# Kernel optimization log

Hardware: AMD Instinct MI355X
Metric: run time of the kernel (lower is better)

Reference implementation:

```python
import jax, jax.numpy as jnp
import numpy as np

# model geometry (matches init_kwargs cfg)
D = 768        # D_EMB
PATCH = 16
T = 8192
N = T // PATCH # 512 patch tokens
H = 12         # heads
HD = D // H    # 64 head dim
NL = 6         # layers
DFF = 4 * D
B = 8
LN_EPS = 1e-5


def setup_inputs() -> dict:
    key = jax.random.key(0)
    ks = iter(jax.random.split(key, 32))
    def g(shape, scale=0.02):
        return jax.random.normal(next(ks), shape, jnp.float32) * scale
    return dict(
        x=jax.random.normal(next(ks), (B, T), jnp.float32),
        pp_w=g((D, PATCH)), pp_b=jnp.zeros((D,), jnp.float32),
        pe=g((N, D)),
        ln1_g=jnp.ones((NL, D), jnp.float32), ln1_b=jnp.zeros((NL, D), jnp.float32),
        qkv_w=g((NL, 3 * D, D)), out_w=g((NL, D, D)),
        ln2_g=jnp.ones((NL, D), jnp.float32), ln2_b=jnp.zeros((NL, D), jnp.float32),
        fc1_w=g((NL, DFF, D)), fc2_w=g((NL, D, DFF)),
        lnf_g=jnp.ones((D,), jnp.float32), lnf_b=jnp.zeros((D,), jnp.float32),
        h1_w=g((D // 2, D)), h1_b=jnp.zeros((D // 2,), jnp.float32),
        h2_w=g((2, D // 2)), h2_b=jnp.zeros((2,), jnp.float32),
    )


def _ln(x, g, b):
    m = x.mean(-1, keepdims=True)
    v = ((x - m) ** 2).mean(-1, keepdims=True)
    return (x - m) / jnp.sqrt(v + LN_EPS) * g + b


def reference(x, pp_w, pp_b, pe, ln1_g, ln1_b, qkv_w, out_w,
              ln2_g, ln2_b, fc1_w, fc2_w, lnf_g, lnf_b,
              h1_w, h1_b, h2_w, h2_b):
    Bx = x.shape[0]
    # patch embed: [B, N, PATCH] @ W^T + b -> [B, N, D]
    z = jnp.einsum('bnp,dp->bnd', x[:, :N * PATCH].reshape(Bx, N, PATCH), pp_w) + pp_b
    z = z + pe  # positional embedding (arange indexes whole table)
    mask = jnp.tril(jnp.ones((N, N), dtype=bool))
    for i in range(NL):
        # --- attention (manual causal softmax, dropout=eval/no-op) ---
        h = _ln(z, ln1_g[i], ln1_b[i])
        qkv = jnp.einsum('bnd,ed->bne', h, qkv_w[i])            # [B,N,3D]
        qkv = qkv.reshape(Bx, N, 3, H, HD).transpose(2, 0, 3, 1, 4)
        q, k, v = qkv[0], qkv[1], qkv[2]                         # [B,H,N,HD]
        s = jnp.einsum('bhld,bhmd->bhlm', q, k) / np.sqrt(HD)
        s = jnp.where(mask, s, -jnp.inf)
        a = jax.nn.softmax(s, axis=-1)
        o = jnp.einsum('bhlm,bhmd->bhld', a, v)
        o = o.transpose(0, 2, 1, 3).reshape(Bx, N, D)
        z = z + jnp.einsum('bnd,ed->bne', o, out_w[i])
        # --- FFN (exact gelu, matching F.gelu default) ---
        h = _ln(z, ln2_g[i], ln2_b[i])
        f = jax.nn.gelu(jnp.einsum('bnd,fd->bnf', h, fc1_w[i]), approximate=False)
        z = z + jnp.einsum('bnf,df->bnd', f, fc2_w[i])
    enc = _ln(z, lnf_g, lnf_b).mean(axis=1)                      # [B, D]
    y = jax.nn.relu(enc @ h1_w.T + h1_b)
    return y @ h2_w.T + h2_b                                     # [B, 2]
```

## Files before the change

kernel.cpp:

```cpp
#include <hip/hip_runtime.h>
#include <hip/hip_bf16.h>
#include <math.h>

#define D_EMB 768
#define NPATCH 16
#define NTOK 512
#define NHEAD 12
#define HDIM 64
#define NLAYER 6
#define DFF 3072
#define BATCH 8
#define MTOK (BATCH * NTOK)

typedef __attribute__((ext_vector_type(8))) short bf16x8;
typedef __attribute__((ext_vector_type(8))) ushort u16x8;
typedef __attribute__((ext_vector_type(4))) float f32x4;

__device__ __forceinline__ float bf2f(ushort s) {
    unsigned u = ((unsigned)s) << 16;
    return __builtin_bit_cast(float, u);
}
__device__ __forceinline__ ushort f2bf(float f) {
    unsigned u = __builtin_bit_cast(unsigned, f);
    unsigned r = (u + 0x7FFFu + ((u >> 16) & 1u)) >> 16;
    return (ushort)r;
}

__global__ __launch_bounds__(256)
void f2bf4_kernel(const float* __restrict__ s0, ushort* __restrict__ d0, int n0,
                  const float* __restrict__ s1, ushort* __restrict__ d1, int n1,
                  const float* __restrict__ s2, ushort* __restrict__ d2, int n2,
                  const float* __restrict__ s3, ushort* __restrict__ d3, int n3)
{
    int i = blockIdx.x * 256 + threadIdx.x;
    const float* s; ushort* d; long long off;
    if (i < n0)                { s = s0; d = d0; off = i; }
    else if (i < n0 + n1)      { s = s1; d = d1; off = i - n0; }
    else if (i < n0 + n1 + n2) { s = s2; d = d2; off = i - n0 - n1; }
    else if (i < n0 + n1 + n2 + n3) { s = s3; d = d3; off = i - n0 - n1 - n2; }
    else return;
    float4 v0 = *(const float4*)(s + off * 8);
    float4 v1 = *(const float4*)(s + off * 8 + 4);
    u16x8 o;
    o[0] = f2bf(v0.x); o[1] = f2bf(v0.y); o[2] = f2bf(v0.z); o[3] = f2bf(v0.w);
    o[4] = f2bf(v1.x); o[5] = f2bf(v1.y); o[6] = f2bf(v1.z); o[7] = f2bf(v1.w);
    *(u16x8*)(d + off * 8) = o;
}

__global__ __launch_bounds__(256)
void patch_embed_kernel(const float* __restrict__ x, const float* __restrict__ pw,
                        const float* __restrict__ pb, const float* __restrict__ pe,
                        float* __restrict__ z)
{
    int bn = blockIdx.x;
    int b = bn >> 9, n = bn & 511;
    __shared__ float xs[NPATCH];
    int t = threadIdx.x;
    if (t < NPATCH) xs[t] = x[(size_t)b * 8192 + n * NPATCH + t];
    __syncthreads();
    for (int d = t; d < D_EMB; d += 256) {
        float acc = pb[d] + pe[(size_t)n * D_EMB + d];
        const float* w = pw + (size_t)d * NPATCH;
        #pragma unroll
        for (int p = 0; p < NPATCH; ++p) acc += xs[p] * w[p];
        z[(size_t)bn * D_EMB + d] = acc;
    }
}

__device__ __forceinline__ float block_reduce_sum_256(float v)
{
    __shared__ float lds[4];
    #pragma unroll
    for (int o = 32; o > 0; o >>= 1) v += __shfl_xor(v, o);
    int lane = threadIdx.x & 63, wid = threadIdx.x >> 6;
    __syncthreads();
    if (lane == 0) lds[wid] = v;
    __syncthreads();
    return lds[0] + lds[1] + lds[2] + lds[3];
}

__device__ __forceinline__ void store_val(float* p, float v)  { *p = v; }
__device__ __forceinline__ void store_val(ushort* p, float v) { *p = f2bf(v); }

template<typename OT>
__global__ __launch_bounds__(256)
void ln_kernel(const float* __restrict__ x, const float* __restrict__ g,
               const float* __restrict__ bta, OT* __restrict__ y)
{
    int row = blockIdx.x;
    const float* xr = x + (size_t)row * D_EMB;
    int t = threadIdx.x;
    float vals[3];
    float s = 0.f;
    #pragma unroll
    for (int i = 0; i < 3; ++i) { vals[i] = xr[t + i * 256]; s += vals[i]; }
    float mean = block_reduce_sum_256(s) * (1.0f / D_EMB);
    float ss = 0.f;
    #pragma unroll
    for (int i = 0; i < 3; ++i) { float d = vals[i] - mean; ss += d * d; }
    float var = block_reduce_sum_256(ss) * (1.0f / D_EMB);
    float rstd = rsqrtf(var + 1e-5f);
    #pragma unroll
    for (int i = 0; i < 3; ++i) {
        int d = t + i * 256;
        store_val(y + (size_t)row * D_EMB + d, (vals[i] - mean) * rstd * g[d] + bta[d]);
    }
}

template<typename OT>
__global__ __launch_bounds__(256)
void reduce_ln_kernel(const float* __restrict__ pbuf, float* __restrict__ z,
                      const float* __restrict__ g, const float* __restrict__ bta,
                      OT* __restrict__ y)
{
    int row = blockIdx.x;
    int t = threadIdx.x;
    const float* p0 = pbuf + (size_t)row * D_EMB;
    const float* p1 = pbuf + (size_t)MTOK * D_EMB + (size_t)row * D_EMB;
    float* zr = z + (size_t)row * D_EMB;
    float vals[3];
    float s = 0.f;
    #pragma unroll
    for (int i = 0; i < 3; ++i) {
        int d = t + i * 256;
        float v = zr[d] + p0[d] + p1[d];
        vals[i] = v;
        zr[d] = v;
        s += v;
    }
    float mean = block_reduce_sum_256(s) * (1.0f / D_EMB);
    float ss = 0.f;
    #pragma unroll
    for (int i = 0; i < 3; ++i) { float d = vals[i] - mean; ss += d * d; }
    float var = block_reduce_sum_256(ss) * (1.0f / D_EMB);
    float rstd = rsqrtf(var + 1e-5f);
    #pragma unroll
    for (int i = 0; i < 3; ++i) {
        int d = t + i * 256;
        store_val(y + (size_t)row * D_EMB + d, (vals[i] - mean) * rstd * g[d] + bta[d]);
    }
}

#define STAGE64(buf)                                                               \
    {                                                                              \
        _Pragma("unroll")                                                          \
        for (int j = 0; j < 2; ++j) {                                              \
            __builtin_amdgcn_global_load_lds(                                      \
                (const __attribute__((address_space(1))) unsigned int*)gA[j],      \
                (__attribute__((address_space(3))) unsigned int*)&As[buf][dA[j]],  \
                16, 0, 0);                                                         \
            gA[j] += 64;                                                           \
        }                                                                          \
        _Pragma("unroll")                                                          \
        for (int j = 0; j < 4; ++j) {                                              \
            __builtin_amdgcn_global_load_lds(                                      \
                (const __attribute__((address_space(1))) unsigned int*)gB[j],      \
                (__attribute__((address_space(3))) unsigned int*)&Bs[buf][dB[j]],  \
                16, 0, 0);                                                         \
            gB[j] += 64;                                                           \
        }                                                                          \
    }

#define COMPUTE64(buf)                                                             \
    {                                                                              \
        bf16x8 a0[4], a1[4], b0[2], b1[2];                                         \
        _Pragma("unroll")                                                          \
        for (int m = 0; m < 4; ++m) {                                              \
            a0[m] = *(const bf16x8*)(&As[buf][rA[m] + x0]);                        \
            a1[m] = *(const bf16x8*)(&As[buf][rA[m] + x1]);                        \
        }                                                                          \
        _Pragma("unroll")                                                          \
        for (int n = 0; n < 2; ++n) {                                              \
            b0[n] = *(const bf16x8*)(&Bs[buf][rB[n] + x0]);                        \
            b1[n] = *(const bf16x8*)(&Bs[buf][rB[n] + x1]);                        \
        }                                                                          \
        _Pragma("unroll")                                                          \
        for (int m = 0; m < 4; ++m)                                                \
            _Pragma("unroll")                                                      \
            for (int n = 0; n < 2; ++n)                                            \
                acc[m][n] = __builtin_amdgcn_mfma_f32_16x16x32_bf16(a0[m], b0[n], acc[m][n], 0, 0, 0); \
        _Pragma("unroll")                                                          \
        for (int m = 0; m < 4; ++m)                                                \
            _Pragma("unroll")                                                      \
            for (int n = 0; n < 2; ++n)                                            \
                acc[m][n] = __builtin_amdgcn_mfma_f32_16x16x32_bf16(a1[m], b1[n], acc[m][n], 0, 0, 0); \
    }

template<int EPI, typename OT, bool SPLITK>
__global__ __launch_bounds__(256)
void mfma_gemm(const ushort* __restrict__ A, const ushort* __restrict__ W,
               OT* __restrict__ C, const float* __restrict__ res,
               int N, int K, int lda)
{
    __shared__ ushort As[2][64 * 64];
    __shared__ ushort Bs[2][128 * 64];

    int gx = gridDim.x, gy = gridDim.y;
    int bx = blockIdx.x, by = blockIdx.y;
    int bz = SPLITK ? blockIdx.z : 0;
    if ((gy & 7) == 0) {
        int flat = bx + gx * (by + gy * bz);
        int xcd = flat & 7, j = flat >> 3;
        int ry = gy >> 3;
        by = xcd * ry + (j % ry);
        int rem = j / ry;
        bx = rem % gx;
        bz = rem / gx;
    }
    int bm = by * 64, bn = bx * 128;

    const ushort* Ab = A + (size_t)bz * K;
    const ushort* Wb = W + (size_t)bz * K;
    OT* Cb = C + (SPLITK ? (size_t)bz * ((size_t)gy * 64) * N : 0);

    int tid = threadIdx.x;
    int w = tid >> 6, l = tid & 63;
    int lr = l & 15, lg = l >> 4;
    f32x4 acc[4][2] = {};

    int srow = w * 8 + (l >> 3);
    int pcol = l & 7;
    int lcol8 = (pcol ^ (srow & 7)) << 3;

    const ushort* gA[2]; const ushort* gB[4];
    int dA[2], dB[4];
    #pragma unroll
    for (int j = 0; j < 2; ++j) {
        gA[j] = Ab + (size_t)(bm + j * 32 + srow) * lda + lcol8;
        dA[j] = (j * 32 + srow) * 64 + (pcol << 3);
    }
    #pragma unroll
    for (int j = 0; j < 4; ++j) {
        gB[j] = Wb + (size_t)(bn + j * 32 + srow) * lda + lcol8;
        dB[j] = (j * 32 + srow) * 64 + (pcol << 3);
    }

    int x0 = ((lg ^ (lr & 7)) << 3);
    int x1 = (((4 + lg) ^ (lr & 7)) << 3);
    int rA[4], rB[2];
    #pragma unroll
    for (int m = 0; m < 4; ++m) rA[m] = (m * 16 + lr) * 64;
    #pragma unroll
    for (int n = 0; n < 2; ++n) rB[n] = (w * 32 + n * 16 + lr) * 64;

    const int nk = K >> 6;
    STAGE64(0);
    __syncthreads();
    for (int t = 0; t < nk; t += 2) {
        STAGE64(1);
        COMPUTE64(0);
        __syncthreads();
        if (t + 2 < nk) STAGE64(0);
        COMPUTE64(1);
        __syncthreads();
    }

    int r0 = lg * 4;
    #pragma unroll
    for (int m = 0; m < 4; ++m) {
        #pragma unroll
        for (int n = 0; n < 2; ++n) {
            #pragma unroll
            for (int j = 0; j < 4; ++j) {
                int gm = bm + m * 16 + r0 + j;
                int gn = bn + w * 32 + n * 16 + lr;
                float v = acc[m][n][j];
                if (EPI == 1) v = 0.5f * v * (1.0f + erff(v * 0.70710678118654752f));
                if (EPI == 2) v += res[(size_t)gm * N + gn];
                store_val(Cb + (size_t)gm * N + gn, v);
            }
        }
    }
}

__global__ __launch_bounds__(256)
void attn_mfma_kernel(const ushort* __restrict__ qkv, ushort* __restrict__ o)
{
    int w = threadIdx.x >> 6, l = threadIdx.x & 63;
    int qt = blockIdx.x * 4 + w;
    int h = blockIdx.y, b = blockIdx.z;
    int q0 = qt * 16;
    int lr = l & 15, lg = l >> 4;

    const size_t rs = 3 * D_EMB;
    const ushort* qbase = qkv + ((size_t)(b * NTOK)) * rs + h * HDIM;
    const ushort* kbase = qbase + D_EMB;
    const ushort* vbase = qbase + 2 * D_EMB;

    bf16x8 qf[2];
    qf[0] = *(const bf16x8*)(qbase + (size_t)(q0 + lr) * rs + lg * 8);
    qf[1] = *(const bf16x8*)(qbase + (size_t)(q0 + lr) * rs + 32 + lg * 8);

    f32x4 oacc[4] = {};
    float m_j[4], l_j[4];
    #pragma unroll
    for (int j = 0; j < 4; ++j) { m_j[j] = -1e30f; l_j[j] = 0.f; }

    __shared__ ushort P_lds[4][16][40];

    int ntiles = q0 / 32 + 1;
    for (int mt = 0; mt < ntiles; ++mt) {
        int m0 = mt * 32;
        f32x4 s[2] = {};
        #pragma unroll
        for (int kb = 0; kb < 2; ++kb) {
            const ushort* kr = kbase + (size_t)(m0 + kb * 16 + lr) * rs;
            bf16x8 k0 = *(const bf16x8*)(kr + lg * 8);
            bf16x8 k1 = *(const bf16x8*)(kr + 32 + lg * 8);
            s[kb] = __builtin_amdgcn_mfma_f32_16x16x32_bf16(qf[0], k0, s[kb], 0, 0, 0);
            s[kb] = __builtin_amdgcn_mfma_f32_16x16x32_bf16(qf[1], k1, s[kb], 0, 0, 0);
        }
        bool partial = (m0 + 31 > q0);
        float p[2][4], mx[4];
        #pragma unroll
        for (int j = 0; j < 4; ++j) {
            int qr = q0 + lg * 4 + j;
            float s0 = s[0][j] * 0.125f;
            float s1 = s[1][j] * 0.125f;
            if (partial) {
                if (m0 + lr > qr)      s0 = -1e30f;
                if (m0 + 16 + lr > qr) s1 = -1e30f;
            }
            p[0][j] = s0; p[1][j] = s1;
            float mm = fmaxf(s0, s1);
            mm = fmaxf(mm, __shfl_xor(mm, 1));
            mm = fmaxf(mm, __shfl_xor(mm, 2));
            mm = fmaxf(mm, __shfl_xor(mm, 4));
            mm = fmaxf(mm, __shfl_xor(mm, 8));
            mx[j] = mm;
        }
        #pragma unroll
        for (int j = 0; j < 4; ++j) {
            float mnew = fmaxf(m_j[j], mx[j]);
            float scale = __expf(m_j[j] - mnew);
            float p0 = __expf(p[0][j] - mnew);
            float p1 = __expf(p[1][j] - mnew);
            p[0][j] = p0; p[1][j] = p1;
            float rsum = p0 + p1;
            rsum += __shfl_xor(rsum, 1);
            rsum += __shfl_xor(rsum, 2);
            rsum += __shfl_xor(rsum, 4);
            rsum += __shfl_xor(rsum, 8);
            l_j[j] = l_j[j] * scale + rsum;
            m_j[j] = mnew;
            #pragma unroll
            for (int i = 0; i < 4; ++i) oacc[i][j] *= scale;
        }
        #pragma unroll
        for (int kb = 0; kb < 2; ++kb)
            #pragma unroll
            for (int j = 0; j < 4; ++j)
                P_lds[w][lg * 4 + j][kb * 16 + lr] = f2bf(p[kb][j]);
        asm volatile("s_waitcnt lgkmcnt(0)" ::: "memory");
        bf16x8 pa = *(const bf16x8*)(&P_lds[w][lr][lg * 8]);
        #pragma unroll
        for (int i = 0; i < 4; ++i) {
            bf16x8 vf;
            const ushort* vp = vbase + (size_t)(m0 + lg * 8) * rs + i * 16 + lr;
            #pragma unroll
            for (int j = 0; j < 8; ++j) vf[j] = (short)vp[(size_t)j * rs];
            oacc[i] = __builtin_amdgcn_mfma_f32_16x16x32_bf16(pa, vf, oacc[i], 0, 0, 0);
        }
    }
    #pragma unroll
    for (int i = 0; i < 4; ++i) {
        #pragma unroll
        for (int j = 0; j < 4; ++j) {
            int qr = q0 + lg * 4 + j;
            int d  = i * 16 + lr;
            float v = oacc[i][j] / l_j[j];
            o[((size_t)(b * NTOK + qr)) * D_EMB + h * HDIM + d] = f2bf(v);
        }
    }
}

__global__ void mean_kernel(const float* __restrict__ x, float* __restrict__ enc)
{
    int b = blockIdx.x; int d = threadIdx.x;
    float s = 0.f;
    for (int n = 0; n < NTOK; ++n) s += x[((size_t)(b * NTOK + n)) * D_EMB + d];
    enc[b * D_EMB + d] = s * (1.0f / NTOK);
}

__global__ void head1_kernel(const float* __restrict__ enc, const float* __restrict__ w,
                             const float* __restrict__ bias, float* __restrict__ r)
{
    int b = blockIdx.x; int j = threadIdx.x;
    float acc = bias[j];
    const float* e = enc + b * D_EMB;
    const float* wr = w + (size_t)j * D_EMB;
    for (int k = 0; k < D_EMB; ++k) acc += e[k] * wr[k];
    r[b * 384 + j] = fmaxf(acc, 0.f);
}

__global__ void head2_kernel(const float* __restrict__ r, const float* __restrict__ w,
                             const float* __restrict__ bias, float* __restrict__ out)
{
    int idx = threadIdx.x;
    if (idx >= 16) return;
    int b = idx >> 1, j = idx & 1;
    float acc = bias[j];
    for (int k = 0; k < 384; ++k) acc += r[b * 384 + k] * w[j * 384 + k];
    out[b * 2 + j] = acc;
}

extern "C" void kernel_launch(void* const* d_in, const int* in_sizes, int n_in,
                              void* d_out, int out_size, void* d_ws, size_t ws_size,
                              hipStream_t stream)
{
    const float* x     = (const float*)d_in[0];
    const float* pp_w  = (const float*)d_in[1];
    const float* pp_b  = (const float*)d_in[2];
    const float* pe    = (const float*)d_in[3];
    const float* ln1_g = (const float*)d_in[4];
    const float* ln1_b = (const float*)d_in[5];
    const float* qkv_w = (const float*)d_in[6];
    const float* out_w = (const float*)d_in[7];
    const float* ln2_g = (const float*)d_in[8];
    const float* ln2_b = (const float*)d_in[9];
    const float* fc1_w = (const float*)d_in[10];
    const float* fc2_w = (const float*)d_in[11];
    const float* lnf_g = (const float*)d_in[12];
    const float* lnf_b = (const float*)d_in[13];
    const float* h1_w  = (const float*)d_in[14];
    const float* h1_b  = (const float*)d_in[15];
    const float* h2_w  = (const float*)d_in[16];
    const float* h2_b  = (const float*)d_in[17];
    float* out = (float*)d_out;

    const int nq = 3 * D_EMB * D_EMB, no = D_EMB * D_EMB, nf = DFF * D_EMB;
    const size_t per_layer_w = ((size_t)nq + no + 2 * nf) * 2;

    char* p = (char*)d_ws;
    float*  z      = (float*)p;  p += (size_t)MTOK * D_EMB * 4;
    ushort* big_bf = (ushort*)p; p += (size_t)MTOK * DFF * 2;
    ushort* h_bf   = (ushort*)p; p += (size_t)MTOK * D_EMB * 2;
    float*  pbuf   = (float*)p;  p += (size_t)2 * MTOK * D_EMB * 4;
    float*  enc    = (float*)p;  p += BATCH * D_EMB * 4;
    float*  r1     = (float*)p;  p += BATCH * 384 * 4;
    size_t base_used = (size_t)(p - (char*)d_ws);
    bool full = (ws_size >= base_used + NLAYER * per_layer_w);
    int nlw = full ? NLAYER : 1;
    ushort* wq_bf  = (ushort*)p; p += (size_t)nlw * nq * 2;
    ushort* wo_bf  = (ushort*)p; p += (size_t)nlw * no * 2;
    ushort* wf1_bf = (ushort*)p; p += (size_t)nlw * nf * 2;
    ushort* wf2_bf = (ushort*)p; p += (size_t)nlw * nf * 2;
    float*  lnf_out = (float*)big_bf;

    patch_embed_kernel<<<MTOK, 256, 0, stream>>>(x, pp_w, pp_b, pe, z);

    if (full) {
        long long tq = (long long)NLAYER * nq / 8, to = (long long)NLAYER * no / 8;
        long long tf = (long long)NLAYER * nf / 8;
        long long tot = tq + to + 2 * tf;
        f2bf4_kernel<<<(int)((tot + 255) / 256), 256, 0, stream>>>(
            qkv_w, wq_bf, (int)tq, out_w, wo_bf, (int)to,
            fc1_w, wf1_bf, (int)tf, fc2_w, wf2_bf, (int)tf);
    }

    ln_kernel<ushort><<<MTOK, 256, 0, stream>>>(z, ln1_g, ln1_b, h_bf);

    const int cvt_blocks = (nq / 8 + no / 8 + 2 * (nf / 8) + 255) / 256;

    for (int i = 0; i < NLAYER; ++i) {
        const ushort* wq  = wq_bf  + (full ? (size_t)i * nq : 0);
        const ushort* wo  = wo_bf  + (full ? (size_t)i * no : 0);
        const ushort* wf1 = wf1_bf + (full ? (size_t)i * nf : 0);
        const ushort* wf2 = wf2_bf + (full ? (size_t)i * nf : 0);
        if (!full) {
            f2bf4_kernel<<<cvt_blocks, 256, 0, stream>>>(
                qkv_w + (size_t)i * nq, wq_bf,  nq / 8,
                out_w + (size_t)i * no, wo_bf,  no / 8,
                fc1_w + (size_t)i * nf, wf1_bf, nf / 8,
                fc2_w + (size_t)i * nf, wf2_bf, nf / 8);
        }

        dim3 gq((3 * D_EMB) / 128, MTOK / 64);
        mfma_gemm<0, ushort, false><<<gq, 256, 0, stream>>>(h_bf, wq, big_bf, nullptr,
                                                            3 * D_EMB, D_EMB, D_EMB);

        dim3 ga(NTOK / 64, NHEAD, BATCH);
        attn_mfma_kernel<<<ga, 256, 0, stream>>>(big_bf, h_bf);

        dim3 gp(D_EMB / 128, MTOK / 64);
        mfma_gemm<2, float, false><<<gp, 256, 0, stream>>>(h_bf, wo, z, z,
                                                           D_EMB, D_EMB, D_EMB);

        ln_kernel<ushort><<<MTOK, 256, 0, stream>>>(z, ln2_g + i * D_EMB, ln2_b + i * D_EMB, h_bf);

        dim3 g1(DFF / 128, MTOK / 64);
        mfma_gemm<1, ushort, false><<<g1, 256, 0, stream>>>(h_bf, wf1, big_bf, nullptr,
                                                            DFF, D_EMB, D_EMB);

        dim3 g2(D_EMB / 128, MTOK / 64, 2);
        mfma_gemm<0, float, true><<<g2, 256, 0, stream>>>(big_bf, wf2, pbuf, nullptr,
                                                          D_EMB, DFF / 2, DFF);

        if (i < NLAYER - 1) {
            reduce_ln_kernel<ushort><<<MTOK, 256, 0, stream>>>(
                pbuf, z, ln1_g + (i + 1) * D_EMB, ln1_b + (i + 1) * D_EMB, h_bf);
        } else {
            reduce_ln_kernel<float><<<MTOK, 256, 0, stream>>>(
                pbuf, z, lnf_g, lnf_b, lnf_out);
        }
    }

    mean_kernel<<<BATCH, D_EMB, 0, stream>>>(lnf_out, enc);
    head1_kernel<<<BATCH, 384, 0, stream>>>(enc, h1_w, h1_b, r1);
    head2_kernel<<<1, 64, 0, stream>>>(r1, h2_w, h2_b, out);
}
```

Before: 1.089 ms.

## Stage V tiles via LDS, split-K out-proj with fused reduce-LN, grid-stride weight cast

The attention kernel now copies each 32x64 V tile into a per-wave swizzled LDS buffer with global_load_lds, replacing strided 2-byte global gathers with LDS reads. The output projection switches to a split-K=2 GEMM writing partials, and a fused reduce+LayerNorm kernel replaces the separate residual epilogue and LN. The weight-conversion kernel becomes a fixed 2048-block grid-stride loop handling 4 floats per thread. These cut uncoalesced V traffic and the idle tail of the out-proj grid, at the cost of extra LDS use, a vmcnt wait and partial-buffer round trips.

```diff
diff --git a/kernel.cpp b/kernel.cpp
--- a/kernel.cpp
+++ b/kernel.cpp
@@ -32,19 +32,19 @@
                   const float* __restrict__ s2, ushort* __restrict__ d2, int n2,
                   const float* __restrict__ s3, ushort* __restrict__ d3, int n3)
 {
-    int i = blockIdx.x * 256 + threadIdx.x;
-    const float* s; ushort* d; long long off;
-    if (i < n0)                { s = s0; d = d0; off = i; }
-    else if (i < n0 + n1)      { s = s1; d = d1; off = i - n0; }
-    else if (i < n0 + n1 + n2) { s = s2; d = d2; off = i - n0 - n1; }
-    else if (i < n0 + n1 + n2 + n3) { s = s3; d = d3; off = i - n0 - n1 - n2; }
-    else return;
-    float4 v0 = *(const float4*)(s + off * 8);
-    float4 v1 = *(const float4*)(s + off * 8 + 4);
-    u16x8 o;
-    o[0] = f2bf(v0.x); o[1] = f2bf(v0.y); o[2] = f2bf(v0.z); o[3] = f2bf(v0.w);
-    o[4] = f2bf(v1.x); o[5] = f2bf(v1.y); o[6] = f2bf(v1.z); o[7] = f2bf(v1.w);
-    *(u16x8*)(d + off * 8) = o;
+    int tot = n0 + n1 + n2 + n3;
+    int stride = gridDim.x * 256;
+    for (int i = blockIdx.x * 256 + threadIdx.x; i < tot; i += stride) {
+        const float* s; ushort* d; int off;
+        if (i < n0)                { s = s0; d = d0; off = i; }
+        else if (i < n0 + n1)      { s = s1; d = d1; off = i - n0; }
+        else if (i < n0 + n1 + n2) { s = s2; d = d2; off = i - n0 - n1; }
+        else                       { s = s3; d = d3; off = i - n0 - n1 - n2; }
+        float4 v = *(const float4*)(s + (size_t)off * 4);
+        ushort4 o;
+        o.x = f2bf(v.x); o.y = f2bf(v.y); o.z = f2bf(v.z); o.w = f2bf(v.w);
+        *(ushort4*)(d + (size_t)off * 4) = o;
+    }
 }
 
 __global__ __launch_bounds__(256)
@@ -296,11 +296,22 @@
     #pragma unroll
     for (int j = 0; j < 4; ++j) { m_j[j] = -1e30f; l_j[j] = 0.f; }
 
+    __shared__ ushort V_lds[4][32 * 64];
     __shared__ ushort P_lds[4][16][40];
 
     int ntiles = q0 / 32 + 1;
     for (int mt = 0; mt < ntiles; ++mt) {
         int m0 = mt * 32;
+        #pragma unroll
+        for (int is = 0; is < 4; ++is) {
+            int row = is * 8 + (l >> 3);
+            int colel = ((l & 7) * 8) ^ (is * 16);
+            const ushort* sv = vbase + (size_t)(m0 + row) * rs + colel;
+            __builtin_amdgcn_global_load_lds(
+                (const __attribute__((address_space(1))) unsigned int*)sv,
+                (__attribute__((address_space(3))) unsigned int*)&V_lds[w][is * 512 + l * 8],
+                16, 0, 0);
+        }
         f32x4 s[2] = {};
         #pragma unroll
         for (int kb = 0; kb < 2; ++kb) {
@@ -353,12 +364,13 @@
                 P_lds[w][lg * 4 + j][kb * 16 + lr] = f2bf(p[kb][j]);
         asm volatile("s_waitcnt lgkmcnt(0)" ::: "memory");
         bf16x8 pa = *(const bf16x8*)(&P_lds[w][lr][lg * 8]);
+        asm volatile("s_waitcnt vmcnt(0)" ::: "memory");
         #pragma unroll
         for (int i = 0; i < 4; ++i) {
             bf16x8 vf;
-            const ushort* vp = vbase + (size_t)(m0 + lg * 8) * rs + i * 16 + lr;
             #pragma unroll
-            for (int j = 0; j < 8; ++j) vf[j] = (short)vp[(size_t)j * rs];
+            for (int j = 0; j < 8; ++j)
+                vf[j] = (short)V_lds[w][(lg * 8 + j) * 64 + ((i * 16 + lr) ^ (lg * 16))];
             oacc[i] = __builtin_amdgcn_mfma_f32_16x16x32_bf16(pa, vf, oacc[i], 0, 0, 0);
         }
     }
@@ -450,17 +462,14 @@
     patch_embed_kernel<<<MTOK, 256, 0, stream>>>(x, pp_w, pp_b, pe, z);
 
     if (full) {
-        long long tq = (long long)NLAYER * nq / 8, to = (long long)NLAYER * no / 8;
-        long long tf = (long long)NLAYER * nf / 8;
-        long long tot = tq + to + 2 * tf;
-        f2bf4_kernel<<<(int)((tot + 255) / 256), 256, 0, stream>>>(
+        long long tq = (long long)NLAYER * nq / 4, to = (long long)NLAYER * no / 4;
+        long long tf = (long long)NLAYER * nf / 4;
+        f2bf4_kernel<<<2048, 256, 0, stream>>>(
             qkv_w, wq_bf, (int)tq, out_w, wo_bf, (int)to,
             fc1_w, wf1_bf, (int)tf, fc2_w, wf2_bf, (int)tf);
     }
 
     ln_kernel<ushort><<<MTOK, 256, 0, stream>>>(z, ln1_g, ln1_b, h_bf);
-
-    const int cvt_blocks = (nq / 8 + no / 8 + 2 * (nf / 8) + 255) / 256;
 
     for (int i = 0; i < NLAYER; ++i) {
         const ushort* wq  = wq_bf  + (full ? (size_t)i * nq : 0);
@@ -468,11 +477,11 @@
         const ushort* wf1 = wf1_bf + (full ? (size_t)i * nf : 0);
         const ushort* wf2 = wf2_bf + (full ? (size_t)i * nf : 0);
         if (!full) {
-            f2bf4_kernel<<<cvt_blocks, 256, 0, stream>>>(
-                qkv_w + (size_t)i * nq, wq_bf,  nq / 8,
-                out_w + (size_t)i * no, wo_bf,  no / 8,
-                fc1_w + (size_t)i * nf, wf1_bf, nf / 8,
-                fc2_w + (size_t)i * nf, wf2_bf, nf / 8);
+            f2bf4_kernel<<<2048, 256, 0, stream>>>(
+                qkv_w + (size_t)i * nq, wq_bf,  nq / 4,
+                out_w + (size_t)i * no, wo_bf,  no / 4,
+                fc1_w + (size_t)i * nf, wf1_bf, nf / 4,
+                fc2_w + (size_t)i * nf, wf2_bf, nf / 4);
         }
 
         dim3 gq((3 * D_EMB) / 128, MTOK / 64);
@@ -482,11 +491,11 @@
         dim3 ga(NTOK / 64, NHEAD, BATCH);
         attn_mfma_kernel<<<ga, 256, 0, stream>>>(big_bf, h_bf);
 
-        dim3 gp(D_EMB / 128, MTOK / 64);
-        mfma_gemm<2, float, false><<<gp, 256, 0, stream>>>(h_bf, wo, z, z,
-                                                           D_EMB, D_EMB, D_EMB);
-
-        ln_kernel<ushort><<<MTOK, 256, 0, stream>>>(z, ln2_g + i * D_EMB, ln2_b + i * D_EMB, h_bf);
+        dim3 gp(D_EMB / 128, MTOK / 64, 2);
+        mfma_gemm<0, float, true><<<gp, 256, 0, stream>>>(h_bf, wo, pbuf, nullptr,
+                                                          D_EMB, D_EMB / 2, D_EMB);
+        reduce_ln_kernel<ushort><<<MTOK, 256, 0, stream>>>(
+            pbuf, z, ln2_g + i * D_EMB, ln2_b + i * D_EMB, h_bf);
 
         dim3 g1(DFF / 128, MTOK / 64);
         mfma_gemm<1, ushort, false><<<g1, 256, 0, stream>>>(h_bf, wf1, big_bf, nullptr,
```

New measurement: 1.107 ms. About the same (+1.7%).
